# Kernel optimization log

Hardware: AMD Instinct MI355X
Metric: run time of the kernel (lower is better)

The kernel has to match this reference:

```python
import jax, jax.numpy as jnp
import numpy as np

N = 50000
EPS = 1e-5

def gcn_conv(x, W, b, edge_index):
    # PyG GCNConv: transform first, then normalized aggregation with self-loops
    xw = x @ W  # [N, out]
    src = jnp.concatenate([edge_index[0], jnp.arange(N)])  # add self-loops
    dst = jnp.concatenate([edge_index[1], jnp.arange(N)])
    deg = jax.ops.segment_sum(jnp.ones_like(dst, dtype=xw.dtype), dst, num_segments=N)
    dis = jnp.where(deg > 0, deg ** -0.5, 0.0)
    norm = dis[src] * dis[dst]  # [E+N]
    out = jax.ops.segment_sum(norm[:, None] * xw[src], dst, num_segments=N)
    return out + b

def batchnorm(x, gamma, beta):
    mean = x.mean(axis=0)
    var = ((x - mean) ** 2).mean(axis=0)  # biased var (training mode)
    return gamma * (x - mean) * jax.lax.rsqrt(var + EPS) + beta

def lrelu(x):
    return jnp.where(x > 0, x, 0.1 * x)

def setup_inputs() -> dict:
    key = jax.random.key(0)
    ks = jax.random.split(key, 12)
    E = 800000
    d = {
        "x": jax.random.normal(ks[0], (N, 3), dtype=jnp.float32),
        "edge_index": jax.random.randint(ks[1], (2, E), 0, N),
        "W1": jax.random.normal(ks[2], (3, 64), dtype=jnp.float32) * (1.0 / np.sqrt(3)),
        "b1": jnp.zeros((64,), jnp.float32),
        "g1": jnp.ones((64,), jnp.float32),
        "be1": jnp.zeros((64,), jnp.float32),
        "W2": jax.random.normal(ks[3], (64, 64), dtype=jnp.float32) * 0.125,
        "b2": jnp.zeros((64,), jnp.float32),
        "g2": jnp.ones((64,), jnp.float32),
        "be2": jnp.zeros((64,), jnp.float32),
        "W3": jax.random.normal(ks[4], (64, 256), dtype=jnp.float32) * 0.125,
        "b3": jnp.zeros((256,), jnp.float32),
        "g3": jnp.ones((256,), jnp.float32),
        "be3": jnp.zeros((256,), jnp.float32),
        "W4": jax.random.normal(ks[5], (256, 1), dtype=jnp.float32) * (1.0 / 16.0),
        "b4": jnp.zeros((1,), jnp.float32),
    }
    return d

def reference(x, edge_index, W1, b1, g1, be1, W2, b2, g2, be2, W3, b3, g3, be3, W4, b4):
    h = lrelu(batchnorm(gcn_conv(x, W1, b1, edge_index), g1, be1))
    h = lrelu(batchnorm(gcn_conv(h, W2, b2, edge_index), g2, be2))
    h = lrelu(batchnorm(gcn_conv(h, W3, b3, edge_index), g3, be3))
    h = gcn_conv(h, W4, b4, edge_index)
    return jax.nn.sigmoid(h)
```

## Files before the change

kernel.cpp:

```cpp
#include <hip/hip_runtime.h>
#include <math.h>

#define NN 50000
#define NP 50048
#define NB (NP / 64)
#define SCAN_NB ((NN + 255) / 256)
#define NBKT ((NN + 255) / 256)

typedef unsigned short u16;
typedef unsigned int u32;

typedef __bf16 bf16x8 __attribute__((ext_vector_type(8)));
typedef float f32x4 __attribute__((ext_vector_type(4)));

__device__ __forceinline__ u16 f2bf(float f) {
    u32 u = __float_as_uint(f);
    u32 r = (u + 0x7FFFu + ((u >> 16) & 1u)) >> 16;
    return (u16)r;
}
__device__ __forceinline__ float bf2f_lo(u32 v) { return __uint_as_float(v << 16); }
__device__ __forceinline__ float bf2f_hi(u32 v) { return __uint_as_float(v & 0xFFFF0000u); }

__global__ __launch_bounds__(256) void k_binA(const int* __restrict__ dst, int E,
                                              int* __restrict__ bcntT, int nblk) {
    __shared__ int h[NBKT];
    for (int i = threadIdx.x; i < NBKT; i += 256) h[i] = 0;
    __syncthreads();
    int base = blockIdx.x * 4096;
#pragma unroll
    for (int i = 0; i < 16; i++) {
        int e = base + i * 256 + threadIdx.x;
        if (e < E) atomicAdd(&h[dst[e] >> 8], 1);
    }
    __syncthreads();
    for (int i = threadIdx.x; i < NBKT; i += 256) bcntT[i * nblk + blockIdx.x] = h[i];
}

__global__ __launch_bounds__(256) void k_binT(const int* __restrict__ bcntT,
        int* __restrict__ colpre, int* __restrict__ tot, int nblk) {
    __shared__ int sh[256];
    int k = blockIdx.x, t = threadIdx.x;
    int v = (t < nblk) ? bcntT[k * nblk + t] : 0;
    sh[t] = v; __syncthreads();
    int inc = v;
    for (int o = 1; o < 256; o <<= 1) {
        int p = (t >= o) ? sh[t - o] : 0;
        __syncthreads();
        inc += p; sh[t] = inc;
        __syncthreads();
    }
    if (t < nblk) colpre[k * nblk + t] = inc - v;
    if (t == 255) tot[k] = inc;
}

__global__ __launch_bounds__(256) void k_scan_tot(const int* __restrict__ tot,
                                                  int* __restrict__ bstart, int E) {
    __shared__ int sh[256];
    int t = threadIdx.x;
    int v = (t < NBKT) ? tot[t] : 0;
    sh[t] = v; __syncthreads();
    int inc = v;
    for (int o = 1; o < 256; o <<= 1) {
        int p = (t >= o) ? sh[t - o] : 0;
        __syncthreads();
        inc += p; sh[t] = inc;
        __syncthreads();
    }
    if (t < NBKT) bstart[t] = inc - v;
    if (t == NBKT - 1) bstart[NBKT] = E;
}

__global__ __launch_bounds__(256) void k_binB(const int* __restrict__ src,
        const int* __restrict__ dst, int E, const int* __restrict__ bstart,
        const int* __restrict__ colpre, int nblk, u32* __restrict__ ebuf) {
    __shared__ int h[NBKT];
    __shared__ int base[NBKT];
    int b = blockIdx.x;
    for (int i = threadIdx.x; i < NBKT; i += 256) {
        h[i] = 0;
        base[i] = bstart[i] + colpre[i * nblk + b];
    }
    __syncthreads();
    int bb = b * 4096;
#pragma unroll
    for (int i = 0; i < 16; i++) {
        int e = bb + i * 256 + threadIdx.x;
        if (e < E) {
            int d = dst[e];
            int k = d >> 8;
            int r = atomicAdd(&h[k], 1);
            ebuf[base[k] + r] = ((u32)d << 16) | (u32)src[e];
        }
    }
}

__global__ __launch_bounds__(256) void k_bcnt(const u32* __restrict__ ebuf,
        const int* __restrict__ bstart, int* __restrict__ cnt, int n) {
    __shared__ int h[256];
    int k = blockIdx.x;
    h[threadIdx.x] = 0; __syncthreads();
    int beg = bstart[k], end = bstart[k + 1];
    for (int j = beg + threadIdx.x; j < end; j += 256)
        atomicAdd(&h[(ebuf[j] >> 16) & 255], 1);
    __syncthreads();
    int r = k * 256 + threadIdx.x;
    if (r < n) cnt[r] = h[threadIdx.x];
}

__global__ __launch_bounds__(256) void k_bfill(const u32* __restrict__ ebuf,
        const int* __restrict__ bstart, const int* __restrict__ rowstart,
        u16* __restrict__ adj, int n) {
    __shared__ int cur[256];
    int k = blockIdx.x;
    int r = k * 256 + threadIdx.x;
    cur[threadIdx.x] = (r < n) ? rowstart[r] : 0;
    __syncthreads();
    int beg = bstart[k], end = bstart[k + 1];
    for (int j = beg + threadIdx.x; j < end; j += 256) {
        u32 e = ebuf[j];
        int p = atomicAdd(&cur[(e >> 16) & 255], 1);
        adj[p] = (u16)(e & 0xFFFF);
    }
}

__global__ void k_bsum_dis(const int* __restrict__ cnt, int* __restrict__ bsum,
                           float* __restrict__ dis, int n) {
    __shared__ int sh[256];
    int i = blockIdx.x * 256 + threadIdx.x;
    int c = (i < n) ? cnt[i] : 0;
    if (i < n) dis[i] = rsqrtf((float)c + 1.0f);
    sh[threadIdx.x] = c;
    __syncthreads();
    for (int off = 128; off; off >>= 1) {
        if (threadIdx.x < off) sh[threadIdx.x] += sh[threadIdx.x + off];
        __syncthreads();
    }
    if (threadIdx.x == 0) bsum[blockIdx.x] = sh[0];
}

__global__ void k_scan_bsum(int* __restrict__ bsum, int nb) {
    __shared__ int sh[256];
    int t = threadIdx.x;
    int v0 = (t < nb) ? bsum[t] : 0;
    sh[t] = v0; __syncthreads();
    int inc = v0;
    for (int off = 1; off < 256; off <<= 1) {
        int o = (t >= off) ? sh[t - off] : 0;
        __syncthreads();
        inc += o; sh[t] = inc;
        __syncthreads();
    }
    if (t < nb) bsum[t] = inc - v0;
}

__global__ void k_scanfin_pre(const int* __restrict__ cnt, const int* __restrict__ bpre,
                              int* __restrict__ rowstart,
                              const float* __restrict__ x, const float* __restrict__ dis,
                              float* __restrict__ p0, int n, int E) {
    __shared__ int sh[256];
    int b = blockIdx.x, t = threadIdx.x;
    int i = b * 256 + t;
    int v0 = (i < n) ? cnt[i] : 0;
    sh[t] = v0; __syncthreads();
    int inc = v0;
    for (int off = 1; off < 256; off <<= 1) {
        int o = (t >= off) ? sh[t - off] : 0;
        __syncthreads();
        inc += o; sh[t] = inc;
        __syncthreads();
    }
    if (i < n) {
        rowstart[i] = bpre[b] + inc - v0;
        float dv = dis[i];
        ((float4*)p0)[i] = make_float4(dv * x[i * 3], dv * x[i * 3 + 1], dv * x[i * 3 + 2], 0.f);
    }
    if (b == gridDim.x - 1 && t == 0) rowstart[n] = E;
}

__global__ void k_wprep_all(const float* __restrict__ W2, const float* __restrict__ W3,
                            u16* __restrict__ w2h, u16* __restrict__ w2l,
                            u16* __restrict__ w3h, u16* __restrict__ w3l) {
    int idx = blockIdx.x * 256 + threadIdx.x;
    float w; u16* ph; u16* pl; int slot;
    if (idx < 64 * 64) {
        int o = idx >> 6, k = idx & 63;
        w = W2[k * 64 + o]; ph = w2h; pl = w2l; slot = o * 64 + k;
    } else if (idx < 64 * 64 + 256 * 64) {
        int i2 = idx - 64 * 64;
        int o = i2 >> 6, k = i2 & 63;
        w = W3[k * 256 + o]; ph = w3h; pl = w3l; slot = o * 64 + k;
    } else return;
    u16 h = f2bf(w);
    float hf = __uint_as_float((u32)h << 16);
    ph[slot] = h;
    pl[slot] = f2bf(w - hf);
}

__global__ void k_gather3(const int* __restrict__ rowstart, const u16* __restrict__ adj,
                          const float* __restrict__ p0, const float* __restrict__ dis,
                          float* __restrict__ z, int n) {
    int row = blockIdx.x * 256 + threadIdx.x;
    if (row >= n) return;
    const float4* P4 = (const float4*)p0;
    float4 v = P4[row];
    float a0 = v.x, a1 = v.y, a2 = v.z;
    int beg = rowstart[row], end = rowstart[row + 1];
    for (int j = beg; j < end; j++) {
        int s = (int)__builtin_nontemporal_load(adj + j);
        float4 w = P4[s];
        a0 += w.x; a1 += w.y; a2 += w.z;
    }
    float dv = dis[row];
    z[row * 3] = dv * a0; z[row * 3 + 1] = dv * a1; z[row * 3 + 2] = dv * a2;
}

__global__ __launch_bounds__(256) void k_gather64_bf16(const int* __restrict__ rowstart,
        const u16* __restrict__ adj, const u16* __restrict__ pb,
        const float* __restrict__ dis, u16* __restrict__ zb, int n) {
    int row = blockIdx.x * 16 + (threadIdx.x >> 4);
    int lane = threadIdx.x & 15;
    if (row >= n) return;
    uint2 v = *((const uint2*)(pb + ((size_t)row << 6)) + lane);
    float a0 = bf2f_lo(v.x), a1 = bf2f_hi(v.x), a2 = bf2f_lo(v.y), a3 = bf2f_hi(v.y);
    int beg = rowstart[row], end = rowstart[row + 1];
    int j = beg;
    for (; j + 3 < end; j += 4) {
        int s0 = (int)__builtin_nontemporal_load(adj + j);
        int s1 = (int)__builtin_nontemporal_load(adj + j + 1);
        int s2 = (int)__builtin_nontemporal_load(adj + j + 2);
        int s3 = (int)__builtin_nontemporal_load(adj + j + 3);
        uint2 v0 = *((const uint2*)(pb + ((size_t)s0 << 6)) + lane);
        uint2 v1 = *((const uint2*)(pb + ((size_t)s1 << 6)) + lane);
        uint2 v2 = *((const uint2*)(pb + ((size_t)s2 << 6)) + lane);
        uint2 v3 = *((const uint2*)(pb + ((size_t)s3 << 6)) + lane);
        a0 += (bf2f_lo(v0.x) + bf2f_lo(v1.x)) + (bf2f_lo(v2.x) + bf2f_lo(v3.x));
        a1 += (bf2f_hi(v0.x) + bf2f_hi(v1.x)) + (bf2f_hi(v2.x) + bf2f_hi(v3.x));
        a2 += (bf2f_lo(v0.y) + bf2f_lo(v1.y)) + (bf2f_lo(v2.y) + bf2f_lo(v3.y));
        a3 += (bf2f_hi(v0.y) + bf2f_hi(v1.y)) + (bf2f_hi(v2.y) + bf2f_hi(v3.y));
    }
    for (; j < end; j++) {
        int s = (int)__builtin_nontemporal_load(adj + j);
        uint2 v0 = *((const uint2*)(pb + ((size_t)s << 6)) + lane);
        a0 += bf2f_lo(v0.x); a1 += bf2f_hi(v0.x);
        a2 += bf2f_lo(v0.y); a3 += bf2f_hi(v0.y);
    }
    float dv = dis[row];
    uint2 o;
    o.x = (u32)f2bf(a0 * dv) | ((u32)f2bf(a1 * dv) << 16);
    o.y = (u32)f2bf(a2 * dv) | ((u32)f2bf(a3 * dv) << 16);
    ((uint2*)(zb + ((size_t)row << 6)))[lane] = o;
}

__global__ void k_gather1_final(const int* __restrict__ rowstart, const u16* __restrict__ adj,
                                const float* __restrict__ q, const float* __restrict__ dis,
                                const float* __restrict__ b4, float* __restrict__ out, int n) {
    int row = blockIdx.x * 256 + threadIdx.x;
    if (row >= n) return;
    float acc = q[row];
    int beg = rowstart[row], end = rowstart[row + 1];
    for (int j = beg; j < end; j++)
        acc += q[(int)__builtin_nontemporal_load(adj + j)];
    float v = dis[row] * acc + b4[0];
    out[row] = 1.f / (1.f + expf(-v));
}

__global__ __launch_bounds__(256) void k_mgemm(const u16* __restrict__ zb,
        const u16* __restrict__ wth, const u16* __restrict__ wtl,
        u16* __restrict__ t, int tstride,
        double* __restrict__ pS, double* __restrict__ pQ) {
    const int wv = threadIdx.x >> 6, lane = threadIdx.x & 63;
    const int lc = lane & 15, lk = lane >> 4;
    const int r0 = blockIdx.x * 64;
    const int col = blockIdx.y * 64 + wv * 16 + lc;

    const bf16x8* wh = (const bf16x8*)(wth + (size_t)col * 64 + lk * 8);
    const bf16x8* wl = (const bf16x8*)(wtl + (size_t)col * 64 + lk * 8);
    bf16x8 bh0 = wh[0], bh1 = wh[4];
    bf16x8 bl0 = wl[0], bl1 = wl[4];

    f32x4 acc[4] = {};
#pragma unroll
    for (int rt = 0; rt < 4; rt++) {
        const bf16x8* ap = (const bf16x8*)(zb + (size_t)(r0 + rt * 16 + lc) * 64 + lk * 8);
        bf16x8 a0 = ap[0], a1 = ap[4];
        acc[rt] = __builtin_amdgcn_mfma_f32_16x16x32_bf16(a0, bh0, acc[rt], 0, 0, 0);
        acc[rt] = __builtin_amdgcn_mfma_f32_16x16x32_bf16(a1, bh1, acc[rt], 0, 0, 0);
        acc[rt] = __builtin_amdgcn_mfma_f32_16x16x32_bf16(a0, bl0, acc[rt], 0, 0, 0);
        acc[rt] = __builtin_amdgcn_mfma_f32_16x16x32_bf16(a1, bl1, acc[rt], 0, 0, 0);
    }
#pragma unroll
    for (int rt = 0; rt < 4; rt++) {
        int rowb = r0 + rt * 16 + lk * 4;
#pragma unroll
        for (int rg = 0; rg < 4; rg++)
            t[(size_t)(rowb + rg) * tstride + col] = f2bf(acc[rt][rg]);
    }
    float s = 0.f, q = 0.f;
#pragma unroll
    for (int rt = 0; rt < 4; rt++)
#pragma unroll
        for (int rg = 0; rg < 4; rg++) { float v = acc[rt][rg]; s += v; q += v * v; }
    s += __shfl_xor(s, 16); q += __shfl_xor(q, 16);
    s += __shfl_xor(s, 32); q += __shfl_xor(q, 32);
    if (lane < 16) {
        pS[(size_t)col * NB + blockIdx.x] = (double)s;
        pQ[(size_t)col * NB + blockIdx.x] = (double)q;
    }
}

__global__ __launch_bounds__(256) void k_gemm3_stats(const float* __restrict__ z,
        const float* __restrict__ W, u16* __restrict__ t,
        double* __restrict__ pS, double* __restrict__ pQ, int n) {
    __shared__ float sH[64 * 4];
    __shared__ float sW[3 * 64];
    __shared__ double red[2 * 16 * 64];
    const int tid = threadIdx.x;
    const int r0 = blockIdx.x * 64;
    for (int i = tid; i < 192; i += 256) {
        int r = i / 3, c = i - r * 3;
        sH[r * 4 + c] = (r0 + r < n) ? z[(size_t)(r0 + r) * 3 + c] : 0.f;
    }
    if (tid < 48) ((float4*)sW)[tid] = ((const float4*)W)[tid];
    __syncthreads();
    const int tx = tid & 15, ty = tid >> 4;
    float4 acc[4];
#pragma unroll
    for (int r = 0; r < 4; r++) acc[r] = make_float4(0.f, 0.f, 0.f, 0.f);
    const float4* sW4 = (const float4*)sW;
#pragma unroll
    for (int k = 0; k < 3; k++) {
        float4 wv = sW4[k * 16 + tx];
#pragma unroll
        for (int r = 0; r < 4; r++) {
            float hs = sH[(ty * 4 + r) * 4 + k];
            acc[r].x += hs * wv.x; acc[r].y += hs * wv.y;
            acc[r].z += hs * wv.z; acc[r].w += hs * wv.w;
        }
    }
#pragma unroll
    for (int r = 0; r < 4; r++) {
        int row = r0 + ty * 4 + r;
        if (row < n) {
            uint2 o;
            o.x = (u32)f2bf(acc[r].x) | ((u32)f2bf(acc[r].y) << 16);
            o.y = (u32)f2bf(acc[r].z) | ((u32)f2bf(acc[r].w) << 16);
            *(uint2*)&t[(size_t)row * 64 + tx * 4] = o;
        }
    }
    double* redS = red;
    double* redQ = red + 16 * 64;
    double s0 = 0, s1 = 0, s2 = 0, s3 = 0, q0 = 0, q1 = 0, q2 = 0, q3 = 0;
#pragma unroll
    for (int r = 0; r < 4; r++) {
        s0 += acc[r].x; q0 += (double)acc[r].x * acc[r].x;
        s1 += acc[r].y; q1 += (double)acc[r].y * acc[r].y;
        s2 += acc[r].z; q2 += (double)acc[r].z * acc[r].z;
        s3 += acc[r].w; q3 += (double)acc[r].w * acc[r].w;
    }
    int base = ty * 64 + tx * 4;
    redS[base + 0] = s0; redS[base + 1] = s1; redS[base + 2] = s2; redS[base + 3] = s3;
    redQ[base + 0] = q0; redQ[base + 1] = q1; redQ[base + 2] = q2; redQ[base + 3] = q3;
    __syncthreads();
    if (ty == 0) {
#pragma unroll
        for (int jj = 0; jj < 4; jj++) {
            int c = tx * 4 + jj;
            double S = 0, Q = 0;
            for (int g = 0; g < 16; g++) { S += redS[g * 64 + c]; Q += redQ[g * 64 + c]; }
            pS[(size_t)c * NB + blockIdx.x] = S;
            pQ[(size_t)c * NB + blockIdx.x] = Q;
        }
    }
}

template<int F>
__global__ __launch_bounds__(256) void k_stats_fin(const double* __restrict__ pS,
        const double* __restrict__ pQ, const float* __restrict__ g,
        const float* __restrict__ be, double* __restrict__ st, int n) {
    __shared__ double shS[256], shQ[256];
    int c = blockIdx.x, t = threadIdx.x;
    double s = 0, q = 0;
    for (int i = t; i < NB; i += 256) {
        s += pS[(size_t)c * NB + i];
        q += pQ[(size_t)c * NB + i];
    }
    shS[t] = s; shQ[t] = q;
    __syncthreads();
    for (int off = 128; off; off >>= 1) {
        if (t < off) { shS[t] += shS[t + off]; shQ[t] += shQ[t + off]; }
        __syncthreads();
    }
    if (t == 0) {
        double mean = shS[0] / n;
        double var = shQ[0] / n - mean * mean;
        if (var < 0.0) var = 0.0;
        double mult = (double)g[c] / sqrt(var + 1e-5);
        st[2 * F + c] = mult;
        st[3 * F + c] = (double)be[c] - mult * mean;
    }
}

__global__ void k_apply64(const u16* __restrict__ t, const float* __restrict__ dis,
                          const double* __restrict__ st, u16* __restrict__ p, int n) {
    int idx = blockIdx.x * 256 + threadIdx.x;
    if (idx >= n * 16) return;
    int row = idx >> 4, c = (idx & 15) * 4;
    uint2 v = ((const uint2*)t)[idx];
    float f0 = bf2f_lo(v.x), f1 = bf2f_hi(v.x), f2 = bf2f_lo(v.y), f3 = bf2f_hi(v.y);
    float m0 = (float)st[128 + c], m1 = (float)st[129 + c],
          m2 = (float)st[130 + c], m3 = (float)st[131 + c];
    float a0 = (float)st[192 + c], a1 = (float)st[193 + c],
          a2 = (float)st[194 + c], a3 = (float)st[195 + c];
    float r0 = m0 * f0 + a0; r0 = r0 > 0.f ? r0 : 0.1f * r0;
    float r1 = m1 * f1 + a1; r1 = r1 > 0.f ? r1 : 0.1f * r1;
    float r2 = m2 * f2 + a2; r2 = r2 > 0.f ? r2 : 0.1f * r2;
    float r3 = m3 * f3 + a3; r3 = r3 > 0.f ? r3 : 0.1f * r3;
    float dv = dis[row];
    uint2 o;
    o.x = (u32)f2bf(r0 * dv) | ((u32)f2bf(r1 * dv) << 16);
    o.y = (u32)f2bf(r2 * dv) | ((u32)f2bf(r3 * dv) << 16);
    ((uint2*)p)[idx] = o;
}

__global__ void k_apply3_dot(const u16* __restrict__ t, const double* __restrict__ st,
                             const float* __restrict__ dis, const float* __restrict__ W4,
                             float* __restrict__ q, int n) {
    int row = blockIdx.x * 4 + (threadIdx.x >> 6);
    int lane = threadIdx.x & 63;
    if (row >= n) return;
    uint2 v = ((const uint2*)t)[(size_t)row * 64 + lane];
    float f0 = bf2f_lo(v.x), f1 = bf2f_hi(v.x), f2 = bf2f_lo(v.y), f3 = bf2f_hi(v.y);
    int c = lane * 4;
    float m0 = (float)st[512 + c], m1 = (float)st[513 + c],
          m2 = (float)st[514 + c], m3 = (float)st[515 + c];
    float a0 = (float)st[768 + c], a1 = (float)st[769 + c],
          a2 = (float)st[770 + c], a3 = (float)st[771 + c];
    float b0 = m0 * f0 + a0; b0 = b0 > 0.f ? b0 : 0.1f * b0;
    float b1 = m1 * f1 + a1; b1 = b1 > 0.f ? b1 : 0.1f * b1;
    float b2 = m2 * f2 + a2; b2 = b2 > 0.f ? b2 : 0.1f * b2;
    float b3 = m3 * f3 + a3; b3 = b3 > 0.f ? b3 : 0.1f * b3;
    float4 w = ((const float4*)W4)[lane];
    float s = b0 * w.x + b1 * w.y + b2 * w.z + b3 * w.w;
#pragma unroll
    for (int off = 32; off; off >>= 1) s += __shfl_down(s, off);
    if (lane == 0) q[row] = dis[row] * s;
}

extern "C" void kernel_launch(void* const* d_in, const int* in_sizes, int n_in,
                              void* d_out, int out_size, void* d_ws, size_t ws_size,
                              hipStream_t stream) {
    const float* x  = (const float*)d_in[0];
    const int*   ei = (const int*)d_in[1];
    const int E = in_sizes[1] / 2;
    const int* src = ei;
    const int* dst = ei + E;
    const float* W1 = (const float*)d_in[2];
    const float* g1 = (const float*)d_in[4];
    const float* be1= (const float*)d_in[5];
    const float* W2 = (const float*)d_in[6];
    const float* g2 = (const float*)d_in[8];
    const float* be2= (const float*)d_in[9];
    const float* W3 = (const float*)d_in[10];
    const float* g3 = (const float*)d_in[12];
    const float* be3= (const float*)d_in[13];
    const float* W4 = (const float*)d_in[14];
    const float* b4 = (const float*)d_in[15];
    float* out = (float*)d_out;

    const int nblk = (E + 4095) / 4096;

    u16*   T    = (u16*)d_ws;
    u16*   P    = T + (size_t)NP * 256;
    u16*   Zb   = P + (size_t)NN * 64;
    u16*   Wt2h = Zb + (size_t)NP * 64;
    u16*   Wt2l = Wt2h + 64 * 64;
    u16*   Wt3h = Wt2l + 64 * 64;
    u16*   Wt3l = Wt3h + 256 * 64;
    double* st  = (double*)(Wt3l + 256 * 64);
    double *st0 = st, *st1 = st + 1024, *st2 = st + 2048;
    double* pS  = st + 3 * 1024;
    double* pQ  = pS + (size_t)256 * NB;
    float* Z3   = (float*)(pQ + (size_t)256 * NB);
    float* P0   = Z3 + NN * 3;
    float* Q    = P0 + NN * 4;
    float* dis  = Q + NN;
    int* cnt      = (int*)(dis + NN);
    int* rowstart = cnt + NN;
    u16* adj      = (u16*)(rowstart + NN + 8);
    int* bsum     = (int*)(adj + E + (E & 1));
    u32* ebuf     = (u32*)(bsum + SCAN_NB + 4);
    int* bcntT    = (int*)(ebuf + E);
    int* colpre   = bcntT + NBKT * nblk;
    int* tot      = colpre + NBKT * nblk;
    int* bstart   = tot + NBKT + 4;

    hipMemsetAsync(Zb + (size_t)NN * 64, 0, (size_t)(NP - NN) * 64 * sizeof(u16), stream);

    k_binA<<<nblk, 256, 0, stream>>>(dst, E, bcntT, nblk);
    k_binT<<<NBKT, 256, 0, stream>>>(bcntT, colpre, tot, nblk);
    k_scan_tot<<<1, 256, 0, stream>>>(tot, bstart, E);
    k_binB<<<nblk, 256, 0, stream>>>(src, dst, E, bstart, colpre, nblk, ebuf);
    k_bcnt<<<NBKT, 256, 0, stream>>>(ebuf, bstart, cnt, NN);
    k_bsum_dis<<<SCAN_NB, 256, 0, stream>>>(cnt, bsum, dis, NN);
    k_scan_bsum<<<1, 256, 0, stream>>>(bsum, SCAN_NB);
    k_scanfin_pre<<<SCAN_NB, 256, 0, stream>>>(cnt, bsum, rowstart, x, dis, P0, NN, E);
    k_bfill<<<NBKT, 256, 0, stream>>>(ebuf, bstart, rowstart, adj, NN);
    k_wprep_all<<<(64 * 64 + 256 * 64 + 255) / 256, 256, 0, stream>>>(W2, W3, Wt2h, Wt2l, Wt3h, Wt3l);

    const int rows_grid = (NN + 255) / 256;
    const int g16_grid  = (NN + 15) / 16;
    const int wave4_grid = (NN + 3) / 4;
    const int app_grid = (NN * 16 + 255) / 256;

    k_gather3<<<rows_grid, 256, 0, stream>>>(rowstart, adj, P0, dis, Z3, NN);
    k_gemm3_stats<<<NB, 256, 0, stream>>>(Z3, W1, T, pS, pQ, NN);
    k_stats_fin<64><<<64, 256, 0, stream>>>(pS, pQ, g1, be1, st0, NN);
    k_apply64<<<app_grid, 256, 0, stream>>>(T, dis, st0, P, NN);

    k_gather64_bf16<<<g16_grid, 256, 0, stream>>>(rowstart, adj, P, dis, Zb, NN);
    k_mgemm<<<dim3(NB, 1), 256, 0, stream>>>(Zb, Wt2h, Wt2l, T, 64, pS, pQ);
    k_stats_fin<64><<<64, 256, 0, stream>>>(pS, pQ, g2, be2, st1, NN);
    k_apply64<<<app_grid, 256, 0, stream>>>(T, dis, st1, P, NN);

    k_gather64_bf16<<<g16_grid, 256, 0, stream>>>(rowstart, adj, P, dis, Zb, NN);
    k_mgemm<<<dim3(NB, 4), 256, 0, stream>>>(Zb, Wt3h, Wt3l, T, 256, pS, pQ);
    k_stats_fin<256><<<256, 256, 0, stream>>>(pS, pQ, g3, be3, st2, NN);

    k_apply3_dot<<<wave4_grid, 256, 0, stream>>>(T, st2, dis, W4, Q, NN);
    k_gather1_final<<<rows_grid, 256, 0, stream>>>(rowstart, adj, Q, dis, b4, out, NN);
}
```

Measured before the change: 198.3 us.

## Sort rows by degree for gathers and fuse CSR build kernels

Builds a degree histogram and a counting-sort permutation of rows by in-degree, so the gather kernels handle rows with similar degree in the same wavefront. This targets divergence and load imbalance from variable-length neighbor loops. It also merges the count, block-sum, degree-inverse, scan and fill kernels, cutting the number of launches. In exchange, gathers read row ids through the permutation, lose coalescing on the per-row output writes, and depend on a global atomic histogram.

```diff
diff --git a/kernel.cpp b/kernel.cpp
--- a/kernel.cpp
+++ b/kernel.cpp
@@ -94,51 +94,36 @@
     }
 }
 
-__global__ __launch_bounds__(256) void k_bcnt(const u32* __restrict__ ebuf,
-        const int* __restrict__ bstart, int* __restrict__ cnt, int n) {
+__global__ __launch_bounds__(256) void k_bcnt_bsum_dis(const u32* __restrict__ ebuf,
+        const int* __restrict__ bstart, int* __restrict__ cnt, float* __restrict__ dis,
+        int* __restrict__ bsum, int* __restrict__ dhist, int n) {
     __shared__ int h[256];
-    int k = blockIdx.x;
-    h[threadIdx.x] = 0; __syncthreads();
+    __shared__ int red[256];
+    int k = blockIdx.x, t = threadIdx.x;
+    h[t] = 0; __syncthreads();
     int beg = bstart[k], end = bstart[k + 1];
-    for (int j = beg + threadIdx.x; j < end; j += 256)
+    for (int j = beg + t; j < end; j += 256)
         atomicAdd(&h[(ebuf[j] >> 16) & 255], 1);
     __syncthreads();
-    int r = k * 256 + threadIdx.x;
-    if (r < n) cnt[r] = h[threadIdx.x];
-}
-
-__global__ __launch_bounds__(256) void k_bfill(const u32* __restrict__ ebuf,
-        const int* __restrict__ bstart, const int* __restrict__ rowstart,
-        u16* __restrict__ adj, int n) {
-    __shared__ int cur[256];
-    int k = blockIdx.x;
-    int r = k * 256 + threadIdx.x;
-    cur[threadIdx.x] = (r < n) ? rowstart[r] : 0;
-    __syncthreads();
-    int beg = bstart[k], end = bstart[k + 1];
-    for (int j = beg + threadIdx.x; j < end; j += 256) {
-        u32 e = ebuf[j];
-        int p = atomicAdd(&cur[(e >> 16) & 255], 1);
-        adj[p] = (u16)(e & 0xFFFF);
-    }
-}
-
-__global__ void k_bsum_dis(const int* __restrict__ cnt, int* __restrict__ bsum,
-                           float* __restrict__ dis, int n) {
-    __shared__ int sh[256];
-    int i = blockIdx.x * 256 + threadIdx.x;
-    int c = (i < n) ? cnt[i] : 0;
-    if (i < n) dis[i] = rsqrtf((float)c + 1.0f);
-    sh[threadIdx.x] = c;
-    __syncthreads();
+    int r = k * 256 + t;
+    int d = h[t];
+    bool valid = (r < n);
+    if (valid) { cnt[r] = d; dis[r] = rsqrtf((float)d + 1.0f); }
+    red[t] = valid ? d : 0;
+    __syncthreads();
+    h[t] = 0; __syncthreads();
+    if (valid) atomicAdd(&h[min(d, 255)], 1);
+    __syncthreads();
+    if (h[t] > 0) atomicAdd(&dhist[t], h[t]);
     for (int off = 128; off; off >>= 1) {
-        if (threadIdx.x < off) sh[threadIdx.x] += sh[threadIdx.x + off];
-        __syncthreads();
-    }
-    if (threadIdx.x == 0) bsum[blockIdx.x] = sh[0];
-}
-
-__global__ void k_scan_bsum(int* __restrict__ bsum, int nb) {
+        if (t < off) red[t] += red[t + off];
+        __syncthreads();
+    }
+    if (t == 0) bsum[k] = red[0];
+}
+
+__global__ __launch_bounds__(256) void k_scan_bsum_dhist(int* __restrict__ bsum, int nb,
+        const int* __restrict__ dhist, int* __restrict__ dcur) {
     __shared__ int sh[256];
     int t = threadIdx.x;
     int v0 = (t < nb) ? bsum[t] : 0;
@@ -151,13 +136,27 @@
         __syncthreads();
     }
     if (t < nb) bsum[t] = inc - v0;
-}
-
-__global__ void k_scanfin_pre(const int* __restrict__ cnt, const int* __restrict__ bpre,
-                              int* __restrict__ rowstart,
-                              const float* __restrict__ x, const float* __restrict__ dis,
-                              float* __restrict__ p0, int n, int E) {
+    __syncthreads();
+    int w0 = dhist[t];
+    sh[t] = w0; __syncthreads();
+    int winc = w0;
+    for (int off = 1; off < 256; off <<= 1) {
+        int o = (t >= off) ? sh[t - off] : 0;
+        __syncthreads();
+        winc += o; sh[t] = winc;
+        __syncthreads();
+    }
+    dcur[t] = winc - w0;
+}
+
+__global__ __launch_bounds__(256) void k_sfpb(const int* __restrict__ cnt,
+        const int* __restrict__ bpre, int* __restrict__ rowstart,
+        const float* __restrict__ x, const float* __restrict__ dis,
+        float* __restrict__ p0, const u32* __restrict__ ebuf,
+        const int* __restrict__ bstart, u16* __restrict__ adj,
+        int* __restrict__ dcur, int* __restrict__ perm, int n, int E) {
     __shared__ int sh[256];
+    __shared__ int cur[256];
     int b = blockIdx.x, t = threadIdx.x;
     int i = b * 256 + t;
     int v0 = (i < n) ? cnt[i] : 0;
@@ -169,12 +168,23 @@
         inc += o; sh[t] = inc;
         __syncthreads();
     }
+    int rs = bpre[b] + inc - v0;
     if (i < n) {
-        rowstart[i] = bpre[b] + inc - v0;
+        rowstart[i] = rs;
         float dv = dis[i];
         ((float4*)p0)[i] = make_float4(dv * x[i * 3], dv * x[i * 3 + 1], dv * x[i * 3 + 2], 0.f);
+        int pos = atomicAdd(&dcur[min(v0, 255)], 1);
+        perm[pos] = i;
     }
     if (b == gridDim.x - 1 && t == 0) rowstart[n] = E;
+    cur[t] = rs;
+    __syncthreads();
+    int beg = bstart[b], end = bstart[b + 1];
+    for (int j = beg + t; j < end; j += 256) {
+        u32 e = ebuf[j];
+        int p = atomicAdd(&cur[(e >> 16) & 255], 1);
+        adj[p] = (u16)(e & 0xFFFF);
+    }
 }
 
 __global__ void k_wprep_all(const float* __restrict__ W2, const float* __restrict__ W3,
@@ -196,11 +206,12 @@
     pl[slot] = f2bf(w - hf);
 }
 
-__global__ void k_gather3(const int* __restrict__ rowstart, const u16* __restrict__ adj,
-                          const float* __restrict__ p0, const float* __restrict__ dis,
-                          float* __restrict__ z, int n) {
-    int row = blockIdx.x * 256 + threadIdx.x;
-    if (row >= n) return;
+__global__ void k_gather3(const int* __restrict__ perm, const int* __restrict__ rowstart,
+                          const u16* __restrict__ adj, const float* __restrict__ p0,
+                          const float* __restrict__ dis, float* __restrict__ z, int n) {
+    int gid = blockIdx.x * 256 + threadIdx.x;
+    if (gid >= n) return;
+    int row = perm[gid];
     const float4* P4 = (const float4*)p0;
     float4 v = P4[row];
     float a0 = v.x, a1 = v.y, a2 = v.z;
@@ -214,12 +225,14 @@
     z[row * 3] = dv * a0; z[row * 3 + 1] = dv * a1; z[row * 3 + 2] = dv * a2;
 }
 
-__global__ __launch_bounds__(256) void k_gather64_bf16(const int* __restrict__ rowstart,
-        const u16* __restrict__ adj, const u16* __restrict__ pb,
-        const float* __restrict__ dis, u16* __restrict__ zb, int n) {
-    int row = blockIdx.x * 16 + (threadIdx.x >> 4);
+__global__ __launch_bounds__(256) void k_gather64_bf16(const int* __restrict__ perm,
+        const int* __restrict__ rowstart, const u16* __restrict__ adj,
+        const u16* __restrict__ pb, const float* __restrict__ dis,
+        u16* __restrict__ zb, int n) {
+    int gid = blockIdx.x * 16 + (threadIdx.x >> 4);
     int lane = threadIdx.x & 15;
-    if (row >= n) return;
+    if (gid >= n) return;
+    int row = perm[gid];
     uint2 v = *((const uint2*)(pb + ((size_t)row << 6)) + lane);
     float a0 = bf2f_lo(v.x), a1 = bf2f_hi(v.x), a2 = bf2f_lo(v.y), a3 = bf2f_hi(v.y);
     int beg = rowstart[row], end = rowstart[row + 1];
@@ -251,11 +264,13 @@
     ((uint2*)(zb + ((size_t)row << 6)))[lane] = o;
 }
 
-__global__ void k_gather1_final(const int* __restrict__ rowstart, const u16* __restrict__ adj,
-                                const float* __restrict__ q, const float* __restrict__ dis,
-                                const float* __restrict__ b4, float* __restrict__ out, int n) {
-    int row = blockIdx.x * 256 + threadIdx.x;
-    if (row >= n) return;
+__global__ void k_gather1_final(const int* __restrict__ perm, const int* __restrict__ rowstart,
+                                const u16* __restrict__ adj, const float* __restrict__ q,
+                                const float* __restrict__ dis, const float* __restrict__ b4,
+                                float* __restrict__ out, int n) {
+    int gid = blockIdx.x * 256 + threadIdx.x;
+    if (gid >= n) return;
+    int row = perm[gid];
     float acc = q[row];
     int beg = rowstart[row], end = rowstart[row + 1];
     for (int j = beg; j < end; j++)
@@ -486,25 +501,28 @@
     float* dis  = Q + NN;
     int* cnt      = (int*)(dis + NN);
     int* rowstart = cnt + NN;
-    u16* adj      = (u16*)(rowstart + NN + 8);
+    int* perm     = rowstart + NN + 8;
+    u16* adj      = (u16*)(perm + NN);
     int* bsum     = (int*)(adj + E + (E & 1));
     u32* ebuf     = (u32*)(bsum + SCAN_NB + 4);
     int* bcntT    = (int*)(ebuf + E);
     int* colpre   = bcntT + NBKT * nblk;
     int* tot      = colpre + NBKT * nblk;
     int* bstart   = tot + NBKT + 4;
+    int* dhist    = bstart + NBKT + 4;
+    int* dcur     = dhist + 256;
 
     hipMemsetAsync(Zb + (size_t)NN * 64, 0, (size_t)(NP - NN) * 64 * sizeof(u16), stream);
+    hipMemsetAsync(dhist, 0, 256 * sizeof(int), stream);
 
     k_binA<<<nblk, 256, 0, stream>>>(dst, E, bcntT, nblk);
     k_binT<<<NBKT, 256, 0, stream>>>(bcntT, colpre, tot, nblk);
     k_scan_tot<<<1, 256, 0, stream>>>(tot, bstart, E);
     k_binB<<<nblk, 256, 0, stream>>>(src, dst, E, bstart, colpre, nblk, ebuf);
-    k_bcnt<<<NBKT, 256, 0, stream>>>(ebuf, bstart, cnt, NN);
-    k_bsum_dis<<<SCAN_NB, 256, 0, stream>>>(cnt, bsum, dis, NN);
-    k_scan_bsum<<<1, 256, 0, stream>>>(bsum, SCAN_NB);
-    k_scanfin_pre<<<SCAN_NB, 256, 0, stream>>>(cnt, bsum, rowstart, x, dis, P0, NN, E);
-    k_bfill<<<NBKT, 256, 0, stream>>>(ebuf, bstart, rowstart, adj, NN);
+    k_bcnt_bsum_dis<<<NBKT, 256, 0, stream>>>(ebuf, bstart, cnt, dis, bsum, dhist, NN);
+    k_scan_bsum_dhist<<<1, 256, 0, stream>>>(bsum, SCAN_NB, dhist, dcur);
+    k_sfpb<<<SCAN_NB, 256, 0, stream>>>(cnt, bsum, rowstart, x, dis, P0, ebuf, bstart,
+                                        adj, dcur, perm, NN, E);
     k_wprep_all<<<(64 * 64 + 256 * 64 + 255) / 256, 256, 0, stream>>>(W2, W3, Wt2h, Wt2l, Wt3h, Wt3l);
 
     const int rows_grid = (NN + 255) / 256;
@@ -512,20 +530,20 @@
     const int wave4_grid = (NN + 3) / 4;
     const int app_grid = (NN * 16 + 255) / 256;
 
-    k_gather3<<<rows_grid, 256, 0, stream>>>(rowstart, adj, P0, dis, Z3, NN);
+    k_gather3<<<rows_grid, 256, 0, stream>>>(perm, rowstart, adj, P0, dis, Z3, NN);
     k_gemm3_stats<<<NB, 256, 0, stream>>>(Z3, W1, T, pS, pQ, NN);
     k_stats_fin<64><<<64, 256, 0, stream>>>(pS, pQ, g1, be1, st0, NN);
     k_apply64<<<app_grid, 256, 0, stream>>>(T, dis, st0, P, NN);
 
-    k_gather64_bf16<<<g16_grid, 256, 0, stream>>>(rowstart, adj, P, dis, Zb, NN);
+    k_gather64_bf16<<<g16_grid, 256, 0, stream>>>(perm, rowstart, adj, P, dis, Zb, NN);
     k_mgemm<<<dim3(NB, 1), 256, 0, stream>>>(Zb, Wt2h, Wt2l, T, 64, pS, pQ);
     k_stats_fin<64><<<64, 256, 0, stream>>>(pS, pQ, g2, be2, st1, NN);
     k_apply64<<<app_grid, 256, 0, stream>>>(T, dis, st1, P, NN);
 
-    k_gather64_bf16<<<g16_grid, 256, 0, stream>>>(rowstart, adj, P, dis, Zb, NN);
+    k_gather64_bf16<<<g16_grid, 256, 0, stream>>>(perm, rowstart, adj, P, dis, Zb, NN);
     k_mgemm<<<dim3(NB, 4), 256, 0, stream>>>(Zb, Wt3h, Wt3l, T, 256, pS, pQ);
     k_stats_fin<256><<<256, 256, 0, stream>>>(pS, pQ, g3, be3, st2, NN);
 
     k_apply3_dot<<<wave4_grid, 256, 0, stream>>>(T, st2, dis, W4, Q, NN);
-    k_gather1_final<<<rows_grid, 256, 0, stream>>>(rowstart, adj, Q, dis, b4, out, NN);
-}
+    k_gather1_final<<<rows_grid, 256, 0, stream>>>(perm, rowstart, adj, Q, dis, b4, out, NN);
+}
```

Result: slower. 355.2 us (+79.1%).
